# Kernel tuning notes

Measured on AMD Instinct MI355X. Metric: run time of the kernel, lower is better.

The kernel has to match this reference:

```python
import jax, jax.numpy as jnp
import numpy as np


def setup_inputs() -> dict:
    key = jax.random.key(0)
    ks = jax.random.split(key, 6)
    B, H, T, Dk, Dv = 64, 16, 4, 128, 256
    q = jax.random.normal(ks[0], (B, H, T, Dk), dtype=jnp.float32)
    k = jax.random.normal(ks[1], (B, H, T, Dk), dtype=jnp.float32)
    v = jax.random.normal(ks[2], (B, H, T, Dv), dtype=jnp.float32)
    g = jax.random.uniform(ks[3], (B, H, T), dtype=jnp.float32)
    beta = jax.random.uniform(ks[4], (B, H, T), dtype=jnp.float32)
    last_recurrent_state = jax.random.normal(ks[5], (B, H, Dk, Dv), dtype=jnp.float32)
    return {"q": q, "k": k, "v": v, "g": g, "beta": beta,
            "last_recurrent_state": last_recurrent_state}


def reference(q, k, v, g, beta, last_recurrent_state):
    # q,k: (B,H,T,Dk)  v: (B,H,T,Dv)  g,beta: (B,H,T)  state: (B,H,Dk,Dv)
    def step(state, xs):
        q_t, k_t, v_t, g_t, beta_t = xs  # (B,H,Dk),(B,H,Dk),(B,H,Dv),(B,H),(B,H)
        state = state * jnp.exp(g_t)[..., None, None]           # decay
        kv_mem = jnp.einsum('bhkv,bhk->bhv', state, k_t)         # readout with key
        delta = (v_t - kv_mem) * beta_t[..., None]               # delta-rule correction
        state = state + k_t[..., None] * delta[..., None, :]     # rank-1 update
        out_t = jnp.einsum('bhkv,bhk->bhv', state, q_t)          # query readout
        return state, out_t

    xs = (jnp.moveaxis(q, 2, 0), jnp.moveaxis(k, 2, 0), jnp.moveaxis(v, 2, 0),
          jnp.moveaxis(g, 2, 0), jnp.moveaxis(beta, 2, 0))
    state, outs = jax.lax.scan(step, last_recurrent_state, xs)
    output = jnp.moveaxis(outs, 0, 2)  # (B,H,T,Dv)
    return jnp.concatenate([output.reshape(-1), state.reshape(-1)], axis=0)
```

## Files before the change

### kernel.cpp

```cpp
#include <hip/hip_runtime.h>

#define BH 1024
#define TT 4
#define DK 128
#define DV 256
#define NW 4
#define RPW 32
#define CH 128

__global__ __launch_bounds__(256)
void delta_rule_kernel(const float* __restrict__ q,
                       const float* __restrict__ k,
                       const float* __restrict__ v,
                       const float* __restrict__ g,
                       const float* __restrict__ beta,
                       const float* __restrict__ s0,
                       float* __restrict__ out)
{
    const int bh   = blockIdx.x >> 1;
    const int half = blockIdx.x & 1;
    const int tid  = threadIdx.x;
    const int w    = tid >> 6;
    const int l    = tid & 63;
    const int col  = half * CH + (l << 1);
    const int lc   = l << 1;
    const int r0   = w * RPW;

    const float* __restrict__ sin_p = s0 + (size_t)bh * DK * DV;
    float* __restrict__ out_p  = out + (size_t)bh * TT * DV;
    float* __restrict__ sout_p = out + (size_t)BH * TT * DV + (size_t)bh * DK * DV;

    const float* __restrict__ kbase = k    + (size_t)bh * TT * DK;
    const float* __restrict__ qbase = q    + (size_t)bh * TT * DK;
    const float* __restrict__ vbase = v    + (size_t)bh * TT * DV;
    const float* __restrict__ gbase = g    + (size_t)bh * TT;
    const float* __restrict__ bbase = beta + (size_t)bh * TT;

    __shared__ __align__(16) float ksh[DK][4];
    __shared__ __align__(16) float qsh[DK][4];
    __shared__ __align__(16) float red[TT][NW][CH];

    const int e0 = tid, e1 = tid + 256;
    const float kl0 = kbase[e0], kl1 = kbase[e1];
    const float ql0 = qbase[e0], ql1 = qbase[e1];

    const float4 gq = *(const float4*)&gbase[0];
    const float4 bq = *(const float4*)&bbase[0];
    float2 va[TT];
#pragma unroll
    for (int t = 0; t < TT; ++t)
        va[t] = *(const float2*)&vbase[t * DV + col];

    float2 s2[RPW];
#pragma unroll
    for (int i = 0; i < RPW; ++i)
        s2[i] = *(const float2*)&sin_p[(size_t)(r0 + i) * DV + col];

    ksh[e0 & 127][e0 >> 7] = kl0;
    ksh[e1 & 127][e1 >> 7] = kl1;
    qsh[e0 & 127][e0 >> 7] = ql0;
    qsh[e1 & 127][e1 >> 7] = ql1;
    __syncthreads();

    const float y0 = expf(gq.x), y1 = expf(gq.y), y2 = expf(gq.z), y3 = expf(gq.w);
    const float G0 = y0, G1 = y0*y1, G2 = y0*y1*y2, G3 = y0*y1*y2*y3;
    const float M01 = y1, M02 = y1*y2, M03 = y1*y2*y3;
    const float M12 = y2, M13 = y2*y3;
    const float M23 = y3;
    const float E = G3;
    const float bt0 = bq.x, bt1 = bq.y, bt2 = bq.z, bt3 = bq.w;

    const float4 kA = *(const float4*)&ksh[l][0];
    const float4 kB = *(const float4*)&ksh[l + 64][0];
    const float4 qA = *(const float4*)&qsh[l][0];
    const float4 qB = *(const float4*)&qsh[l + 64][0];
    const float a0[4] = {kA.x, kA.y, kA.z, kA.w};
    const float a1[4] = {kB.x, kB.y, kB.z, kB.w};
    const float b0[4] = {qA.x, qA.y, qA.z, qA.w};
    const float b1[4] = {qB.x, qB.y, qB.z, qB.w};
    float AA[4][4];
    float BB[4][4];
#pragma unroll
    for (int s = 0; s < 4; ++s) {
#pragma unroll
        for (int t = 0; t < 4; ++t) {
            if (t > s) {
                float x = fmaf(a1[s], a1[t], a0[s] * a0[t]);
#pragma unroll
                for (int m = 1; m < 64; m <<= 1) x += __shfl_xor(x, m);
                AA[s][t] = x;
            }
            if (t >= s) {
                float x = fmaf(a1[s], b1[t], a0[s] * b0[t]);
#pragma unroll
                for (int m = 1; m < 64; m <<= 1) x += __shfl_xor(x, m);
                BB[s][t] = x;
            }
        }
    }

    float2 c[TT] = {{0.f,0.f},{0.f,0.f},{0.f,0.f},{0.f,0.f}};
#pragma unroll
    for (int i = 0; i < RPW; ++i) {
        const float4 k4 = *(const float4*)&ksh[r0 + i][0];
        c[0].x = fmaf(s2[i].x, k4.x, c[0].x); c[0].y = fmaf(s2[i].y, k4.x, c[0].y);
        c[1].x = fmaf(s2[i].x, k4.y, c[1].x); c[1].y = fmaf(s2[i].y, k4.y, c[1].y);
        c[2].x = fmaf(s2[i].x, k4.z, c[2].x); c[2].y = fmaf(s2[i].y, k4.z, c[2].y);
        c[3].x = fmaf(s2[i].x, k4.w, c[3].x); c[3].y = fmaf(s2[i].y, k4.w, c[3].y);
    }
#pragma unroll
    for (int t = 0; t < TT; ++t)
        *(float2*)&red[t][w][lc] = c[t];
    __syncthreads();
#pragma unroll
    for (int t = 0; t < TT; ++t) {
        const float2 u0 = *(const float2*)&red[t][0][lc];
        const float2 u1 = *(const float2*)&red[t][1][lc];
        const float2 u2 = *(const float2*)&red[t][2][lc];
        const float2 u3 = *(const float2*)&red[t][3][lc];
        c[t].x = (u0.x + u1.x) + (u2.x + u3.x);
        c[t].y = (u0.y + u1.y) + (u2.y + u3.y);
    }

    float2 d0, d1, d2, d3;
    d0.x = bt0 * (va[0].x - G0 * c[0].x);
    d0.y = bt0 * (va[0].y - G0 * c[0].y);
    d1.x = bt1 * (va[1].x - G1 * c[1].x - M01 * AA[0][1] * d0.x);
    d1.y = bt1 * (va[1].y - G1 * c[1].y - M01 * AA[0][1] * d0.y);
    d2.x = bt2 * (va[2].x - G2 * c[2].x - M02 * AA[0][2] * d0.x - M12 * AA[1][2] * d1.x);
    d2.y = bt2 * (va[2].y - G2 * c[2].y - M02 * AA[0][2] * d0.y - M12 * AA[1][2] * d1.y);
    d3.x = bt3 * (va[3].x - G3 * c[3].x - M03 * AA[0][3] * d0.x - M13 * AA[1][3] * d1.x - M23 * AA[2][3] * d2.x);
    d3.y = bt3 * (va[3].y - G3 * c[3].y - M03 * AA[0][3] * d0.y - M13 * AA[1][3] * d1.y - M23 * AA[2][3] * d2.y);

    const float W0t = M03, W1t = M13, W2t = M23;
    float2 p[TT] = {{0.f,0.f},{0.f,0.f},{0.f,0.f},{0.f,0.f}};
#pragma unroll
    for (int i = 0; i < RPW; ++i) {
        const int r = r0 + i;
        const float4 k4 = *(const float4*)&ksh[r][0];
        const float4 q4 = *(const float4*)&qsh[r][0];
        const float2 s = s2[i];
        p[0].x = fmaf(s.x, q4.x, p[0].x); p[0].y = fmaf(s.y, q4.x, p[0].y);
        p[1].x = fmaf(s.x, q4.y, p[1].x); p[1].y = fmaf(s.y, q4.y, p[1].y);
        p[2].x = fmaf(s.x, q4.z, p[2].x); p[2].y = fmaf(s.y, q4.z, p[2].y);
        p[3].x = fmaf(s.x, q4.w, p[3].x); p[3].y = fmaf(s.y, q4.w, p[3].y);
        const float h0 = W0t * k4.x, h1 = W1t * k4.y, h2 = W2t * k4.z, h3 = k4.w;
        float nx = s.x * E, ny = s.y * E;
        nx = fmaf(h0, d0.x, nx); ny = fmaf(h0, d0.y, ny);
        nx = fmaf(h1, d1.x, nx); ny = fmaf(h1, d1.y, ny);
        nx = fmaf(h2, d2.x, nx); ny = fmaf(h2, d2.y, ny);
        nx = fmaf(h3, d3.x, nx); ny = fmaf(h3, d3.y, ny);
        *(float2*)&sout_p[(size_t)r * DV + col] = make_float2(nx, ny);
    }

    __syncthreads();
#pragma unroll
    for (int t = 0; t < TT; ++t)
        *(float2*)&red[t][w][lc] = p[t];
    __syncthreads();

    const float2 darr[4] = {d0, d1, d2, d3};
    const float Gt[4] = {G0, G1, G2, G3};
    const float Mm[4][4] = {{1.f, M01, M02, M03},
                            {0.f, 1.f, M12, M13},
                            {0.f, 0.f, 1.f, M23},
                            {0.f, 0.f, 0.f, 1.f}};
#pragma unroll
    for (int t = 0; t < TT; ++t) {
        if (w == t) {
            const float2 u0 = *(const float2*)&red[t][0][lc];
            const float2 u1 = *(const float2*)&red[t][1][lc];
            const float2 u2 = *(const float2*)&red[t][2][lc];
            const float2 u3 = *(const float2*)&red[t][3][lc];
            float ox = Gt[t] * ((u0.x + u1.x) + (u2.x + u3.x));
            float oy = Gt[t] * ((u0.y + u1.y) + (u2.y + u3.y));
#pragma unroll
            for (int s = 0; s < TT; ++s) {
                if (s <= t) {
                    const float cf = Mm[s][t] * BB[s][t];
                    ox = fmaf(cf, darr[s].x, ox);
                    oy = fmaf(cf, darr[s].y, oy);
                }
            }
            *(float2*)&out_p[t * DV + col] = make_float2(ox, oy);
        }
    }
}

extern "C" void kernel_launch(void* const* d_in, const int* in_sizes, int n_in,
                              void* d_out, int out_size, void* d_ws, size_t ws_size,
                              hipStream_t stream) {
    const float* q    = (const float*)d_in[0];
    const float* k    = (const float*)d_in[1];
    const float* v    = (const float*)d_in[2];
    const float* g    = (const float*)d_in[3];
    const float* beta = (const float*)d_in[4];
    const float* s0   = (const float*)d_in[5];
    float* out = (float*)d_out;

    delta_rule_kernel<<<dim3(BH * 2), dim3(256), 0, stream>>>(q, k, v, g, beta, s0, out);
}
```

Before: 248.6 us.

## Persistent blocks process four heads with software-pipelined prefetch of next head

The grid shrinks from 2048 to 512 blocks, and each block now loops over four (batch,head) pairs. During the state-update loop it prefetches the next head's state, k, q, v, g and beta into registers and double-buffered shared memory, so global loads overlap with compute and stores. The cost is higher register pressure, since a second s2 array and extra prefetched values stay live. There are also fewer resident blocks to hide latency, which could lower occupancy on a memory-bound kernel.

```diff
diff --git a/kernel.cpp b/kernel.cpp
--- a/kernel.cpp
+++ b/kernel.cpp
@@ -7,6 +7,8 @@
 #define NW 4
 #define RPW 32
 #define CH 128
+#define NBLK 512
+#define NU 4
 
 __global__ __launch_bounds__(256)
 void delta_rule_kernel(const float* __restrict__ q,
@@ -17,172 +19,207 @@
                        const float* __restrict__ s0,
                        float* __restrict__ out)
 {
-    const int bh   = blockIdx.x >> 1;
-    const int half = blockIdx.x & 1;
+    const int b    = blockIdx.x;
+    const int half = b & 1;
     const int tid  = threadIdx.x;
     const int w    = tid >> 6;
     const int l    = tid & 63;
     const int col  = half * CH + (l << 1);
     const int lc   = l << 1;
     const int r0   = w * RPW;
-
-    const float* __restrict__ sin_p = s0 + (size_t)bh * DK * DV;
-    float* __restrict__ out_p  = out + (size_t)bh * TT * DV;
-    float* __restrict__ sout_p = out + (size_t)BH * TT * DV + (size_t)bh * DK * DV;
-
-    const float* __restrict__ kbase = k    + (size_t)bh * TT * DK;
-    const float* __restrict__ qbase = q    + (size_t)bh * TT * DK;
-    const float* __restrict__ vbase = v    + (size_t)bh * TT * DV;
-    const float* __restrict__ gbase = g    + (size_t)bh * TT;
-    const float* __restrict__ bbase = beta + (size_t)bh * TT;
-
-    __shared__ __align__(16) float ksh[DK][4];
-    __shared__ __align__(16) float qsh[DK][4];
-    __shared__ __align__(16) float red[TT][NW][CH];
-
-    const int e0 = tid, e1 = tid + 256;
-    const float kl0 = kbase[e0], kl1 = kbase[e1];
-    const float ql0 = qbase[e0], ql1 = qbase[e1];
-
-    const float4 gq = *(const float4*)&gbase[0];
-    const float4 bq = *(const float4*)&bbase[0];
+    const int e0   = tid, e1 = tid + 256;
+
+    __shared__ __align__(16) float ksh[2][DK][4];
+    __shared__ __align__(16) float qsh[2][DK][4];
+    __shared__ __align__(16) float redc[TT][NW][CH];
+    __shared__ __align__(16) float redp[TT][NW][CH];
+
+    int bh = b >> 1;
+    {
+        const float* kb = k + (size_t)bh * TT * DK;
+        const float* qb = q + (size_t)bh * TT * DK;
+        const float kl0 = kb[e0], kl1 = kb[e1];
+        const float ql0 = qb[e0], ql1 = qb[e1];
+        ksh[0][e0 & 127][e0 >> 7] = kl0;
+        ksh[0][e1 & 127][e1 >> 7] = kl1;
+        qsh[0][e0 & 127][e0 >> 7] = ql0;
+        qsh[0][e1 & 127][e1 >> 7] = ql1;
+    }
+    float4 gq = *(const float4*)(g    + (size_t)bh * TT);
+    float4 bq = *(const float4*)(beta + (size_t)bh * TT);
     float2 va[TT];
-#pragma unroll
-    for (int t = 0; t < TT; ++t)
-        va[t] = *(const float2*)&vbase[t * DV + col];
-
+    {
+        const float* vb = v + (size_t)bh * TT * DV;
+#pragma unroll
+        for (int t = 0; t < TT; ++t)
+            va[t] = *(const float2*)&vb[t * DV + col];
+    }
     float2 s2[RPW];
-#pragma unroll
-    for (int i = 0; i < RPW; ++i)
-        s2[i] = *(const float2*)&sin_p[(size_t)(r0 + i) * DV + col];
-
-    ksh[e0 & 127][e0 >> 7] = kl0;
-    ksh[e1 & 127][e1 >> 7] = kl1;
-    qsh[e0 & 127][e0 >> 7] = ql0;
-    qsh[e1 & 127][e1 >> 7] = ql1;
+    {
+        const float* sp = s0 + (size_t)bh * DK * DV;
+#pragma unroll
+        for (int i = 0; i < RPW; ++i)
+            s2[i] = *(const float2*)&sp[(size_t)(r0 + i) * DV + col];
+    }
     __syncthreads();
 
-    const float y0 = expf(gq.x), y1 = expf(gq.y), y2 = expf(gq.z), y3 = expf(gq.w);
-    const float G0 = y0, G1 = y0*y1, G2 = y0*y1*y2, G3 = y0*y1*y2*y3;
-    const float M01 = y1, M02 = y1*y2, M03 = y1*y2*y3;
-    const float M12 = y2, M13 = y2*y3;
-    const float M23 = y3;
-    const float E = G3;
-    const float bt0 = bq.x, bt1 = bq.y, bt2 = bq.z, bt3 = bq.w;
-
-    const float4 kA = *(const float4*)&ksh[l][0];
-    const float4 kB = *(const float4*)&ksh[l + 64][0];
-    const float4 qA = *(const float4*)&qsh[l][0];
-    const float4 qB = *(const float4*)&qsh[l + 64][0];
-    const float a0[4] = {kA.x, kA.y, kA.z, kA.w};
-    const float a1[4] = {kB.x, kB.y, kB.z, kB.w};
-    const float b0[4] = {qA.x, qA.y, qA.z, qA.w};
-    const float b1[4] = {qB.x, qB.y, qB.z, qB.w};
-    float AA[4][4];
-    float BB[4][4];
-#pragma unroll
-    for (int s = 0; s < 4; ++s) {
-#pragma unroll
-        for (int t = 0; t < 4; ++t) {
-            if (t > s) {
-                float x = fmaf(a1[s], a1[t], a0[s] * a0[t]);
-#pragma unroll
-                for (int m = 1; m < 64; m <<= 1) x += __shfl_xor(x, m);
-                AA[s][t] = x;
+#pragma unroll
+    for (int u = 0; u < NU; ++u) {
+        const int par = u & 1;
+        const int bhu = (b >> 1) + (u << 8);
+        const int bhn = bhu + 256;
+        float* __restrict__ out_p  = out + (size_t)bhu * TT * DV;
+        float* __restrict__ sout_p = out + (size_t)BH * TT * DV + (size_t)bhu * DK * DV;
+
+        const float y0 = expf(gq.x), y1 = expf(gq.y), y2 = expf(gq.z), y3 = expf(gq.w);
+        const float G0 = y0, G1 = y0*y1, G2 = y0*y1*y2, G3 = y0*y1*y2*y3;
+        const float M01 = y1, M02 = y1*y2, M03 = y1*y2*y3;
+        const float M12 = y2, M13 = y2*y3, M23 = y3;
+        const float E = G3;
+        const float bt0 = bq.x, bt1 = bq.y, bt2 = bq.z, bt3 = bq.w;
+
+        const float4 kA = *(const float4*)&ksh[par][l][0];
+        const float4 kB = *(const float4*)&ksh[par][l + 64][0];
+        const float4 qA = *(const float4*)&qsh[par][l][0];
+        const float4 qB = *(const float4*)&qsh[par][l + 64][0];
+        const float a0[4] = {kA.x, kA.y, kA.z, kA.w};
+        const float a1[4] = {kB.x, kB.y, kB.z, kB.w};
+        const float b0[4] = {qA.x, qA.y, qA.z, qA.w};
+        const float b1[4] = {qB.x, qB.y, qB.z, qB.w};
+        float AA[4][4], BBm[4][4];
+#pragma unroll
+        for (int s = 0; s < 4; ++s) {
+#pragma unroll
+            for (int t = 0; t < 4; ++t) {
+                if (t > s) {
+                    float x = fmaf(a1[s], a1[t], a0[s] * a0[t]);
+#pragma unroll
+                    for (int m = 1; m < 64; m <<= 1) x += __shfl_xor(x, m);
+                    AA[s][t] = x;
+                }
+                if (t >= s) {
+                    float x = fmaf(a1[s], b1[t], a0[s] * b0[t]);
+#pragma unroll
+                    for (int m = 1; m < 64; m <<= 1) x += __shfl_xor(x, m);
+                    BBm[s][t] = x;
+                }
             }
-            if (t >= s) {
-                float x = fmaf(a1[s], b1[t], a0[s] * b0[t]);
-#pragma unroll
-                for (int m = 1; m < 64; m <<= 1) x += __shfl_xor(x, m);
-                BB[s][t] = x;
-            }
-        }
-    }
-
-    float2 c[TT] = {{0.f,0.f},{0.f,0.f},{0.f,0.f},{0.f,0.f}};
-#pragma unroll
-    for (int i = 0; i < RPW; ++i) {
-        const float4 k4 = *(const float4*)&ksh[r0 + i][0];
-        c[0].x = fmaf(s2[i].x, k4.x, c[0].x); c[0].y = fmaf(s2[i].y, k4.x, c[0].y);
-        c[1].x = fmaf(s2[i].x, k4.y, c[1].x); c[1].y = fmaf(s2[i].y, k4.y, c[1].y);
-        c[2].x = fmaf(s2[i].x, k4.z, c[2].x); c[2].y = fmaf(s2[i].y, k4.z, c[2].y);
-        c[3].x = fmaf(s2[i].x, k4.w, c[3].x); c[3].y = fmaf(s2[i].y, k4.w, c[3].y);
-    }
-#pragma unroll
-    for (int t = 0; t < TT; ++t)
-        *(float2*)&red[t][w][lc] = c[t];
-    __syncthreads();
-#pragma unroll
-    for (int t = 0; t < TT; ++t) {
-        const float2 u0 = *(const float2*)&red[t][0][lc];
-        const float2 u1 = *(const float2*)&red[t][1][lc];
-        const float2 u2 = *(const float2*)&red[t][2][lc];
-        const float2 u3 = *(const float2*)&red[t][3][lc];
-        c[t].x = (u0.x + u1.x) + (u2.x + u3.x);
-        c[t].y = (u0.y + u1.y) + (u2.y + u3.y);
-    }
-
-    float2 d0, d1, d2, d3;
-    d0.x = bt0 * (va[0].x - G0 * c[0].x);
-    d0.y = bt0 * (va[0].y - G0 * c[0].y);
-    d1.x = bt1 * (va[1].x - G1 * c[1].x - M01 * AA[0][1] * d0.x);
-    d1.y = bt1 * (va[1].y - G1 * c[1].y - M01 * AA[0][1] * d0.y);
-    d2.x = bt2 * (va[2].x - G2 * c[2].x - M02 * AA[0][2] * d0.x - M12 * AA[1][2] * d1.x);
-    d2.y = bt2 * (va[2].y - G2 * c[2].y - M02 * AA[0][2] * d0.y - M12 * AA[1][2] * d1.y);
-    d3.x = bt3 * (va[3].x - G3 * c[3].x - M03 * AA[0][3] * d0.x - M13 * AA[1][3] * d1.x - M23 * AA[2][3] * d2.x);
-    d3.y = bt3 * (va[3].y - G3 * c[3].y - M03 * AA[0][3] * d0.y - M13 * AA[1][3] * d1.y - M23 * AA[2][3] * d2.y);
-
-    const float W0t = M03, W1t = M13, W2t = M23;
-    float2 p[TT] = {{0.f,0.f},{0.f,0.f},{0.f,0.f},{0.f,0.f}};
-#pragma unroll
-    for (int i = 0; i < RPW; ++i) {
-        const int r = r0 + i;
-        const float4 k4 = *(const float4*)&ksh[r][0];
-        const float4 q4 = *(const float4*)&qsh[r][0];
-        const float2 s = s2[i];
-        p[0].x = fmaf(s.x, q4.x, p[0].x); p[0].y = fmaf(s.y, q4.x, p[0].y);
-        p[1].x = fmaf(s.x, q4.y, p[1].x); p[1].y = fmaf(s.y, q4.y, p[1].y);
-        p[2].x = fmaf(s.x, q4.z, p[2].x); p[2].y = fmaf(s.y, q4.z, p[2].y);
-        p[3].x = fmaf(s.x, q4.w, p[3].x); p[3].y = fmaf(s.y, q4.w, p[3].y);
-        const float h0 = W0t * k4.x, h1 = W1t * k4.y, h2 = W2t * k4.z, h3 = k4.w;
-        float nx = s.x * E, ny = s.y * E;
-        nx = fmaf(h0, d0.x, nx); ny = fmaf(h0, d0.y, ny);
-        nx = fmaf(h1, d1.x, nx); ny = fmaf(h1, d1.y, ny);
-        nx = fmaf(h2, d2.x, nx); ny = fmaf(h2, d2.y, ny);
-        nx = fmaf(h3, d3.x, nx); ny = fmaf(h3, d3.y, ny);
-        *(float2*)&sout_p[(size_t)r * DV + col] = make_float2(nx, ny);
-    }
-
-    __syncthreads();
-#pragma unroll
-    for (int t = 0; t < TT; ++t)
-        *(float2*)&red[t][w][lc] = p[t];
-    __syncthreads();
-
-    const float2 darr[4] = {d0, d1, d2, d3};
-    const float Gt[4] = {G0, G1, G2, G3};
-    const float Mm[4][4] = {{1.f, M01, M02, M03},
-                            {0.f, 1.f, M12, M13},
-                            {0.f, 0.f, 1.f, M23},
-                            {0.f, 0.f, 0.f, 1.f}};
-#pragma unroll
-    for (int t = 0; t < TT; ++t) {
-        if (w == t) {
-            const float2 u0 = *(const float2*)&red[t][0][lc];
-            const float2 u1 = *(const float2*)&red[t][1][lc];
-            const float2 u2 = *(const float2*)&red[t][2][lc];
-            const float2 u3 = *(const float2*)&red[t][3][lc];
+        }
+
+        float2 c[TT] = {{0.f,0.f},{0.f,0.f},{0.f,0.f},{0.f,0.f}};
+#pragma unroll
+        for (int i = 0; i < RPW; ++i) {
+            const float4 k4 = *(const float4*)&ksh[par][r0 + i][0];
+            c[0].x = fmaf(s2[i].x, k4.x, c[0].x); c[0].y = fmaf(s2[i].y, k4.x, c[0].y);
+            c[1].x = fmaf(s2[i].x, k4.y, c[1].x); c[1].y = fmaf(s2[i].y, k4.y, c[1].y);
+            c[2].x = fmaf(s2[i].x, k4.z, c[2].x); c[2].y = fmaf(s2[i].y, k4.z, c[2].y);
+            c[3].x = fmaf(s2[i].x, k4.w, c[3].x); c[3].y = fmaf(s2[i].y, k4.w, c[3].y);
+        }
+#pragma unroll
+        for (int t = 0; t < TT; ++t)
+            *(float2*)&redc[t][w][lc] = c[t];
+        __syncthreads();
+#pragma unroll
+        for (int t = 0; t < TT; ++t) {
+            const float2 u0 = *(const float2*)&redc[t][0][lc];
+            const float2 u1 = *(const float2*)&redc[t][1][lc];
+            const float2 u2 = *(const float2*)&redc[t][2][lc];
+            const float2 u3 = *(const float2*)&redc[t][3][lc];
+            c[t].x = (u0.x + u1.x) + (u2.x + u3.x);
+            c[t].y = (u0.y + u1.y) + (u2.y + u3.y);
+        }
+
+        float2 d0, d1, d2, d3;
+        d0.x = bt0 * (va[0].x - G0 * c[0].x);
+        d0.y = bt0 * (va[0].y - G0 * c[0].y);
+        d1.x = bt1 * (va[1].x - G1 * c[1].x - M01 * AA[0][1] * d0.x);
+        d1.y = bt1 * (va[1].y - G1 * c[1].y - M01 * AA[0][1] * d0.y);
+        d2.x = bt2 * (va[2].x - G2 * c[2].x - M02 * AA[0][2] * d0.x - M12 * AA[1][2] * d1.x);
+        d2.y = bt2 * (va[2].y - G2 * c[2].y - M02 * AA[0][2] * d0.y - M12 * AA[1][2] * d1.y);
+        d3.x = bt3 * (va[3].x - G3 * c[3].x - M03 * AA[0][3] * d0.x - M13 * AA[1][3] * d1.x - M23 * AA[2][3] * d2.x);
+        d3.y = bt3 * (va[3].y - G3 * c[3].y - M03 * AA[0][3] * d0.y - M13 * AA[1][3] * d1.y - M23 * AA[2][3] * d2.y);
+
+        float nkl0, nkl1, nql0, nql1;
+        float4 ngq, nbq;
+        float2 nva[TT];
+        if (u < NU - 1) {
+            const float* kbn = k + (size_t)bhn * TT * DK;
+            const float* qbn = q + (size_t)bhn * TT * DK;
+            nkl0 = kbn[e0]; nkl1 = kbn[e1];
+            nql0 = qbn[e0]; nql1 = qbn[e1];
+            ngq = *(const float4*)(g    + (size_t)bhn * TT);
+            nbq = *(const float4*)(beta + (size_t)bhn * TT);
+            const float* vbn = v + (size_t)bhn * TT * DV;
+#pragma unroll
+            for (int t = 0; t < TT; ++t)
+                nva[t] = *(const float2*)&vbn[t * DV + col];
+        }
+
+        const float W0t = M03, W1t = M13, W2t = M23;
+        const float* __restrict__ spn = s0 + (size_t)bhn * DK * DV;
+        float2 p[TT] = {{0.f,0.f},{0.f,0.f},{0.f,0.f},{0.f,0.f}};
+#pragma unroll
+        for (int i = 0; i < RPW; ++i) {
+            const int r = r0 + i;
+            const float4 k4 = *(const float4*)&ksh[par][r][0];
+            const float4 q4 = *(const float4*)&qsh[par][r][0];
+            const float2 s = s2[i];
+            p[0].x = fmaf(s.x, q4.x, p[0].x); p[0].y = fmaf(s.y, q4.x, p[0].y);
+            p[1].x = fmaf(s.x, q4.y, p[1].x); p[1].y = fmaf(s.y, q4.y, p[1].y);
+            p[2].x = fmaf(s.x, q4.z, p[2].x); p[2].y = fmaf(s.y, q4.z, p[2].y);
+            p[3].x = fmaf(s.x, q4.w, p[3].x); p[3].y = fmaf(s.y, q4.w, p[3].y);
+            const float h0 = W0t * k4.x, h1 = W1t * k4.y, h2 = W2t * k4.z, h3 = k4.w;
+            float nx = s.x * E, ny = s.y * E;
+            nx = fmaf(h0, d0.x, nx); ny = fmaf(h0, d0.y, ny);
+            nx = fmaf(h1, d1.x, nx); ny = fmaf(h1, d1.y, ny);
+            nx = fmaf(h2, d2.x, nx); ny = fmaf(h2, d2.y, ny);
+            nx = fmaf(h3, d3.x, nx); ny = fmaf(h3, d3.y, ny);
+            *(float2*)&sout_p[(size_t)r * DV + col] = make_float2(nx, ny);
+            if (u < NU - 1)
+                s2[i] = *(const float2*)&spn[(size_t)r * DV + col];
+        }
+#pragma unroll
+        for (int t = 0; t < TT; ++t)
+            *(float2*)&redp[t][w][lc] = p[t];
+        __syncthreads();
+
+        if (u < NU - 1) {
+            ksh[par ^ 1][e0 & 127][e0 >> 7] = nkl0;
+            ksh[par ^ 1][e1 & 127][e1 >> 7] = nkl1;
+            qsh[par ^ 1][e0 & 127][e0 >> 7] = nql0;
+            qsh[par ^ 1][e1 & 127][e1 >> 7] = nql1;
+        }
+
+        {
+            const float2 darr[4] = {d0, d1, d2, d3};
+            const float Gt[4] = {G0, G1, G2, G3};
+            const float Mm[4][4] = {{1.f, M01, M02, M03},
+                                    {0.f, 1.f, M12, M13},
+                                    {0.f, 0.f, 1.f, M23},
+                                    {0.f, 0.f, 0.f, 1.f}};
+            const int t = w;
+            const float2 u0 = *(const float2*)&redp[t][0][lc];
+            const float2 u1 = *(const float2*)&redp[t][1][lc];
+            const float2 u2 = *(const float2*)&redp[t][2][lc];
+            const float2 u3 = *(const float2*)&redp[t][3][lc];
             float ox = Gt[t] * ((u0.x + u1.x) + (u2.x + u3.x));
             float oy = Gt[t] * ((u0.y + u1.y) + (u2.y + u3.y));
 #pragma unroll
             for (int s = 0; s < TT; ++s) {
                 if (s <= t) {
-                    const float cf = Mm[s][t] * BB[s][t];
+                    const float cf = Mm[s][t] * BBm[s][t];
                     ox = fmaf(cf, darr[s].x, ox);
                     oy = fmaf(cf, darr[s].y, oy);
                 }
             }
             *(float2*)&out_p[t * DV + col] = make_float2(ox, oy);
+        }
+
+        if (u < NU - 1) {
+            __syncthreads();
+            gq = ngq; bq = nbq;
+#pragma unroll
+            for (int t = 0; t < TT; ++t) va[t] = nva[t];
         }
     }
 }
@@ -198,5 +235,5 @@
     const float* s0   = (const float*)d_in[5];
     float* out = (float*)d_out;
 
-    delta_rule_kernel<<<dim3(BH * 2), dim3(256), 0, stream>>>(q, k, v, g, beta, s0, out);
+    delta_rule_kernel<<<dim3(NBLK), dim3(256), 0, stream>>>(q, k, v, g, beta, s0, out);
 }
```

After: 253.2 us. About the same (+1.8%).

## Split fused delta-rule kernel into readout pass and state-update pass

Applied to the files above, without the earlier changes.

Replaces the single fused kernel with two kernels. The first computes the readouts of the state against k and q with float4 loads over full rows, then computes the delta corrections and outputs and writes the deltas to workspace. The second re-reads the state and the deltas to write the updated state with streaming float4 accesses. This removes the need to hold the state tile in registers across phases and improves memory access width and parallelism, at the cost of reading the state twice plus a second launch.

```diff
diff --git a/kernel.cpp b/kernel.cpp
--- a/kernel.cpp
+++ b/kernel.cpp
@@ -4,71 +4,51 @@
 #define TT 4
 #define DK 128
 #define DV 256
-#define NW 4
-#define RPW 32
-#define CH 128
+#define OUTOFF (BH * TT * DV)
+
+
+#define FMA4(acc, s, kk) \
+    acc.x = fmaf(s.x, kk, acc.x); acc.y = fmaf(s.y, kk, acc.y); \
+    acc.z = fmaf(s.z, kk, acc.z); acc.w = fmaf(s.w, kk, acc.w)
 
 __global__ __launch_bounds__(256)
-void delta_rule_kernel(const float* __restrict__ q,
-                       const float* __restrict__ k,
-                       const float* __restrict__ v,
-                       const float* __restrict__ g,
-                       const float* __restrict__ beta,
-                       const float* __restrict__ s0,
-                       float* __restrict__ out)
+void p1_readout(const float* __restrict__ q, const float* __restrict__ k,
+                const float* __restrict__ v, const float* __restrict__ g,
+                const float* __restrict__ beta, const float* __restrict__ s0,
+                float* __restrict__ out, float* __restrict__ dws)
 {
-    const int bh   = blockIdx.x >> 1;
-    const int half = blockIdx.x & 1;
-    const int tid  = threadIdx.x;
-    const int w    = tid >> 6;
-    const int l    = tid & 63;
-    const int col  = half * CH + (l << 1);
-    const int lc   = l << 1;
-    const int r0   = w * RPW;
+    const int bh  = blockIdx.x;
+    const int tid = threadIdx.x;
+    const int rg  = tid >> 6;
+    const int l   = tid & 63;
+    const int cq  = l << 2;
 
-    const float* __restrict__ sin_p = s0 + (size_t)bh * DK * DV;
-    float* __restrict__ out_p  = out + (size_t)bh * TT * DV;
-    float* __restrict__ sout_p = out + (size_t)BH * TT * DV + (size_t)bh * DK * DV;
-
-    const float* __restrict__ kbase = k    + (size_t)bh * TT * DK;
-    const float* __restrict__ qbase = q    + (size_t)bh * TT * DK;
-    const float* __restrict__ vbase = v    + (size_t)bh * TT * DV;
-    const float* __restrict__ gbase = g    + (size_t)bh * TT;
-    const float* __restrict__ bbase = beta + (size_t)bh * TT;
+    const float* __restrict__ kb = k  + (size_t)bh * TT * DK;
+    const float* __restrict__ qb = q  + (size_t)bh * TT * DK;
+    const float* __restrict__ vb = v  + (size_t)bh * TT * DV;
+    const float* __restrict__ sp = s0 + (size_t)bh * DK * DV;
+    float* __restrict__ out_p = out + (size_t)bh * TT * DV;
+    float* __restrict__ d_p   = dws + (size_t)bh * TT * DV;
 
     __shared__ __align__(16) float ksh[DK][4];
     __shared__ __align__(16) float qsh[DK][4];
-    __shared__ __align__(16) float red[TT][NW][CH];
+    __shared__ __align__(16) float redc[TT][4][DV];
+    __shared__ __align__(16) float redp[TT][4][DV];
 
     const int e0 = tid, e1 = tid + 256;
-    const float kl0 = kbase[e0], kl1 = kbase[e1];
-    const float ql0 = qbase[e0], ql1 = qbase[e1];
-
-    const float4 gq = *(const float4*)&gbase[0];
-    const float4 bq = *(const float4*)&bbase[0];
-    float2 va[TT];
+    const float kl0 = kb[e0], kl1 = kb[e1];
+    const float ql0 = qb[e0], ql1 = qb[e1];
+    float vv[TT];
 #pragma unroll
-    for (int t = 0; t < TT; ++t)
-        va[t] = *(const float2*)&vbase[t * DV + col];
-
-    float2 s2[RPW];
-#pragma unroll
-    for (int i = 0; i < RPW; ++i)
-        s2[i] = *(const float2*)&sin_p[(size_t)(r0 + i) * DV + col];
+    for (int t = 0; t < TT; ++t) vv[t] = vb[t * DV + tid];
+    const float4 gq = *(const float4*)(g    + (size_t)bh * TT);
+    const float4 bq = *(const float4*)(beta + (size_t)bh * TT);
 
     ksh[e0 & 127][e0 >> 7] = kl0;
     ksh[e1 & 127][e1 >> 7] = kl1;
     qsh[e0 & 127][e0 >> 7] = ql0;
     qsh[e1 & 127][e1 >> 7] = ql1;
     __syncthreads();
-
-    const float y0 = expf(gq.x), y1 = expf(gq.y), y2 = expf(gq.z), y3 = expf(gq.w);
-    const float G0 = y0, G1 = y0*y1, G2 = y0*y1*y2, G3 = y0*y1*y2*y3;
-    const float M01 = y1, M02 = y1*y2, M03 = y1*y2*y3;
-    const float M12 = y2, M13 = y2*y3;
-    const float M23 = y3;
-    const float E = G3;
-    const float bt0 = bq.x, bt1 = bq.y, bt2 = bq.z, bt3 = bq.w;
 
     const float4 kA = *(const float4*)&ksh[l][0];
     const float4 kB = *(const float4*)&ksh[l + 64][0];
@@ -78,8 +58,7 @@
     const float a1[4] = {kB.x, kB.y, kB.z, kB.w};
     const float b0[4] = {qA.x, qA.y, qA.z, qA.w};
     const float b1[4] = {qB.x, qB.y, qB.z, qB.w};
-    float AA[4][4];
-    float BB[4][4];
+    float AA[4][4], BB[4][4];
 #pragma unroll
     for (int s = 0; s < 4; ++s) {
 #pragma unroll
@@ -99,91 +78,105 @@
         }
     }
 
-    float2 c[TT] = {{0.f,0.f},{0.f,0.f},{0.f,0.f},{0.f,0.f}};
+    float4 c4[TT] = {{0,0,0,0},{0,0,0,0},{0,0,0,0},{0,0,0,0}};
+    float4 p4[TT] = {{0,0,0,0},{0,0,0,0},{0,0,0,0},{0,0,0,0}};
 #pragma unroll
-    for (int i = 0; i < RPW; ++i) {
-        const float4 k4 = *(const float4*)&ksh[r0 + i][0];
-        c[0].x = fmaf(s2[i].x, k4.x, c[0].x); c[0].y = fmaf(s2[i].y, k4.x, c[0].y);
-        c[1].x = fmaf(s2[i].x, k4.y, c[1].x); c[1].y = fmaf(s2[i].y, k4.y, c[1].y);
-        c[2].x = fmaf(s2[i].x, k4.z, c[2].x); c[2].y = fmaf(s2[i].y, k4.z, c[2].y);
-        c[3].x = fmaf(s2[i].x, k4.w, c[3].x); c[3].y = fmaf(s2[i].y, k4.w, c[3].y);
+    for (int i = 0; i < 32; ++i) {
+        const int r = rg * 32 + i;
+        const float4 s  = *(const float4*)&sp[(size_t)r * DV + cq];
+        const float4 k4 = *(const float4*)&ksh[r][0];
+        const float4 q4 = *(const float4*)&qsh[r][0];
+        FMA4(c4[0], s, k4.x); FMA4(c4[1], s, k4.y);
+        FMA4(c4[2], s, k4.z); FMA4(c4[3], s, k4.w);
+        FMA4(p4[0], s, q4.x); FMA4(p4[1], s, q4.y);
+        FMA4(p4[2], s, q4.z); FMA4(p4[3], s, q4.w);
     }
 #pragma unroll
-    for (int t = 0; t < TT; ++t)
-        *(float2*)&red[t][w][lc] = c[t];
+    for (int t = 0; t < TT; ++t) {
+        *(float4*)&redc[t][rg][cq] = c4[t];
+        *(float4*)&redp[t][rg][cq] = p4[t];
+    }
     __syncthreads();
+
+    const int col = tid;
+    float cc[TT], pp[TT];
 #pragma unroll
     for (int t = 0; t < TT; ++t) {
-        const float2 u0 = *(const float2*)&red[t][0][lc];
-        const float2 u1 = *(const float2*)&red[t][1][lc];
-        const float2 u2 = *(const float2*)&red[t][2][lc];
-        const float2 u3 = *(const float2*)&red[t][3][lc];
-        c[t].x = (u0.x + u1.x) + (u2.x + u3.x);
-        c[t].y = (u0.y + u1.y) + (u2.y + u3.y);
+        cc[t] = (redc[t][0][col] + redc[t][1][col]) + (redc[t][2][col] + redc[t][3][col]);
+        pp[t] = (redp[t][0][col] + redp[t][1][col]) + (redp[t][2][col] + redp[t][3][col]);
     }
+    const float y0 = expf(gq.x), y1 = expf(gq.y), y2 = expf(gq.z), y3 = expf(gq.w);
+    const float G0 = y0, G1 = y0*y1, G2 = y0*y1*y2, G3 = y0*y1*y2*y3;
+    const float M01 = y1, M02 = y1*y2, M03 = y1*y2*y3;
+    const float M12 = y2, M13 = y2*y3, M23 = y3;
 
-    float2 d0, d1, d2, d3;
-    d0.x = bt0 * (va[0].x - G0 * c[0].x);
-    d0.y = bt0 * (va[0].y - G0 * c[0].y);
-    d1.x = bt1 * (va[1].x - G1 * c[1].x - M01 * AA[0][1] * d0.x);
-    d1.y = bt1 * (va[1].y - G1 * c[1].y - M01 * AA[0][1] * d0.y);
-    d2.x = bt2 * (va[2].x - G2 * c[2].x - M02 * AA[0][2] * d0.x - M12 * AA[1][2] * d1.x);
-    d2.y = bt2 * (va[2].y - G2 * c[2].y - M02 * AA[0][2] * d0.y - M12 * AA[1][2] * d1.y);
-    d3.x = bt3 * (va[3].x - G3 * c[3].x - M03 * AA[0][3] * d0.x - M13 * AA[1][3] * d1.x - M23 * AA[2][3] * d2.x);
-    d3.y = bt3 * (va[3].y - G3 * c[3].y - M03 * AA[0][3] * d0.y - M13 * AA[1][3] * d1.y - M23 * AA[2][3] * d2.y);
+    float d0, d1, d2, d3;
+    d0 = bq.x * (vv[0] - G0 * cc[0]);
+    d1 = bq.y * (vv[1] - G1 * cc[1] - M01 * AA[0][1] * d0);
+    d2 = bq.z * (vv[2] - G2 * cc[2] - M02 * AA[0][2] * d0 - M12 * AA[1][2] * d1);
+    d3 = bq.w * (vv[3] - G3 * cc[3] - M03 * AA[0][3] * d0 - M13 * AA[1][3] * d1
+                                     - M23 * AA[2][3] * d2);
 
-    const float W0t = M03, W1t = M13, W2t = M23;
-    float2 p[TT] = {{0.f,0.f},{0.f,0.f},{0.f,0.f},{0.f,0.f}};
+    float o0 = fmaf(BB[0][0], d0, G0 * pp[0]);
+    float o1 = G1 * pp[1];
+    o1 = fmaf(M01 * BB[0][1], d0, o1);
+    o1 = fmaf(BB[1][1], d1, o1);
+    float o2 = G2 * pp[2];
+    o2 = fmaf(M02 * BB[0][2], d0, o2);
+    o2 = fmaf(M12 * BB[1][2], d1, o2);
+    o2 = fmaf(BB[2][2], d2, o2);
+    float o3 = G3 * pp[3];
+    o3 = fmaf(M03 * BB[0][3], d0, o3);
+    o3 = fmaf(M13 * BB[1][3], d1, o3);
+    o3 = fmaf(M23 * BB[2][3], d2, o3);
+    o3 = fmaf(BB[3][3], d3, o3);
+
+    out_p[0 * DV + col] = o0;  out_p[1 * DV + col] = o1;
+    out_p[2 * DV + col] = o2;  out_p[3 * DV + col] = o3;
+    d_p[0 * DV + col] = d0;    d_p[1 * DV + col] = d1;
+    d_p[2 * DV + col] = d2;    d_p[3 * DV + col] = d3;
+}
+
+__global__ __launch_bounds__(256)
+void p2_update(const float* __restrict__ k, const float* __restrict__ g,
+               const float* __restrict__ s0, const float* __restrict__ dws,
+               float* __restrict__ out)
+{
+    const int gw = blockIdx.x * 4 + (threadIdx.x >> 6);
+    const int bh = gw >> 3;
+    const int r0 = (gw & 7) << 4;
+    const int cq = (threadIdx.x & 63) << 2;
+
+    const float4 gq = *(const float4*)(g + (size_t)bh * TT);
+    const float y1 = expf(gq.y), y2 = expf(gq.z), y3 = expf(gq.w);
+    const float y0 = expf(gq.x);
+    const float G3 = y0 * y1 * y2 * y3;
+    const float W0 = y1 * y2 * y3, W1 = y2 * y3, W2 = y3;
+
+    const float* __restrict__ dd = dws + (size_t)bh * TT * DV;
+    const float4 d0 = *(const float4*)&dd[0 * DV + cq];
+    const float4 d1 = *(const float4*)&dd[1 * DV + cq];
+    const float4 d2 = *(const float4*)&dd[2 * DV + cq];
+    const float4 d3 = *(const float4*)&dd[3 * DV + cq];
+
+    const float* __restrict__ kb = k + (size_t)bh * TT * DK;
+    const float* __restrict__ sp = s0 + (size_t)bh * DK * DV;
+    float* __restrict__ so = out + (size_t)OUTOFF + (size_t)bh * DK * DV;
+
 #pragma unroll
-    for (int i = 0; i < RPW; ++i) {
+    for (int i = 0; i < 16; ++i) {
         const int r = r0 + i;
-        const float4 k4 = *(const float4*)&ksh[r][0];
-        const float4 q4 = *(const float4*)&qsh[r][0];
-        const float2 s = s2[i];
-        p[0].x = fmaf(s.x, q4.x, p[0].x); p[0].y = fmaf(s.y, q4.x, p[0].y);
-        p[1].x = fmaf(s.x, q4.y, p[1].x); p[1].y = fmaf(s.y, q4.y, p[1].y);
-        p[2].x = fmaf(s.x, q4.z, p[2].x); p[2].y = fmaf(s.y, q4.z, p[2].y);
-        p[3].x = fmaf(s.x, q4.w, p[3].x); p[3].y = fmaf(s.y, q4.w, p[3].y);
-        const float h0 = W0t * k4.x, h1 = W1t * k4.y, h2 = W2t * k4.z, h3 = k4.w;
-        float nx = s.x * E, ny = s.y * E;
-        nx = fmaf(h0, d0.x, nx); ny = fmaf(h0, d0.y, ny);
-        nx = fmaf(h1, d1.x, nx); ny = fmaf(h1, d1.y, ny);
-        nx = fmaf(h2, d2.x, nx); ny = fmaf(h2, d2.y, ny);
-        nx = fmaf(h3, d3.x, nx); ny = fmaf(h3, d3.y, ny);
-        *(float2*)&sout_p[(size_t)r * DV + col] = make_float2(nx, ny);
-    }
-
-    __syncthreads();
-#pragma unroll
-    for (int t = 0; t < TT; ++t)
-        *(float2*)&red[t][w][lc] = p[t];
-    __syncthreads();
-
-    const float2 darr[4] = {d0, d1, d2, d3};
-    const float Gt[4] = {G0, G1, G2, G3};
-    const float Mm[4][4] = {{1.f, M01, M02, M03},
-                            {0.f, 1.f, M12, M13},
-                            {0.f, 0.f, 1.f, M23},
-                            {0.f, 0.f, 0.f, 1.f}};
-#pragma unroll
-    for (int t = 0; t < TT; ++t) {
-        if (w == t) {
-            const float2 u0 = *(const float2*)&red[t][0][lc];
-            const float2 u1 = *(const float2*)&red[t][1][lc];
-            const float2 u2 = *(const float2*)&red[t][2][lc];
-            const float2 u3 = *(const float2*)&red[t][3][lc];
-            float ox = Gt[t] * ((u0.x + u1.x) + (u2.x + u3.x));
-            float oy = Gt[t] * ((u0.y + u1.y) + (u2.y + u3.y));
-#pragma unroll
-            for (int s = 0; s < TT; ++s) {
-                if (s <= t) {
-                    const float cf = Mm[s][t] * BB[s][t];
-                    ox = fmaf(cf, darr[s].x, ox);
-                    oy = fmaf(cf, darr[s].y, oy);
-                }
-            }
-            *(float2*)&out_p[t * DV + col] = make_float2(ox, oy);
-        }
+        const float h0 = W0 * kb[0 * DK + r];
+        const float h1 = W1 * kb[1 * DK + r];
+        const float h2 = W2 * kb[2 * DK + r];
+        const float h3 =      kb[3 * DK + r];
+        const float4 s = *(const float4*)&sp[(size_t)r * DV + cq];
+        float4 o;
+        o.x = fmaf(h0, d0.x, fmaf(h1, d1.x, fmaf(h2, d2.x, fmaf(h3, d3.x, s.x * G3))));
+        o.y = fmaf(h0, d0.y, fmaf(h1, d1.y, fmaf(h2, d2.y, fmaf(h3, d3.y, s.y * G3))));
+        o.z = fmaf(h0, d0.z, fmaf(h1, d1.z, fmaf(h2, d2.z, fmaf(h3, d3.z, s.z * G3))));
+        o.w = fmaf(h0, d0.w, fmaf(h1, d1.w, fmaf(h2, d2.w, fmaf(h3, d3.w, s.w * G3))));
+        *(float4*)&so[(size_t)r * DV + cq] = o;
     }
 }
 
@@ -197,6 +190,8 @@
     const float* beta = (const float*)d_in[4];
     const float* s0   = (const float*)d_in[5];
     float* out = (float*)d_out;
+    float* dws = (float*)d_ws;
 
-    delta_rule_kernel<<<dim3(BH * 2), dim3(256), 0, stream>>>(q, k, v, g, beta, s0, out);
+    p1_readout<<<dim3(BH), dim3(256), 0, stream>>>(q, k, v, g, beta, s0, out, dws);
+    p2_update <<<dim3(2048), dim3(256), 0, stream>>>(k, g, s0, dws, out);
 }
```

Result: slower. 273.8 us (+10.1%).
